# Optimization experiments

Measured on AMD Instinct MI355X. Metric: run time of the kernel, lower is better.

## Reference

```python
import jax, jax.numpy as jnp
import numpy as np

B, N, DIM = 4, 4096, 768
H = 12
DH = DIM // H          # 64
S = 16                 # num_segments
M = N // S             # 256 segment_len
SCALE = DH ** -0.5


def setup_inputs() -> dict:
    key = jax.random.key(0)
    ks = jax.random.split(key, 7)
    std = DIM ** -0.5
    return {
        "x": jax.random.normal(ks[0], (B, N, DIM), dtype=jnp.float32),
        "Wq": jax.random.normal(ks[1], (DIM, DIM), dtype=jnp.float32) * std,
        "Wkv": jax.random.normal(ks[2], (DIM, DIM), dtype=jnp.float32) * std,
        "Wo": jax.random.normal(ks[3], (DIM, DIM), dtype=jnp.float32) * std,
        "bo": jax.random.normal(ks[4], (DIM,), dtype=jnp.float32) * 0.02,
        "Wo0": jax.random.normal(ks[5], (DIM, DIM), dtype=jnp.float32) * std,
        "bo0": jax.random.normal(ks[6], (DIM,), dtype=jnp.float32) * 0.02,
    }


def _rotary_freqs(n, dh, dtype):
    # lucidrains RotaryEmbedding: inv_freq over even dims, emb = cat(freqs, freqs)
    inv_freq = 1.0 / (10000.0 ** (jnp.arange(0, dh, 2, dtype=jnp.float32) / dh))
    t = jnp.arange(n, dtype=jnp.float32)
    freqs = jnp.einsum("n,f->nf", t, inv_freq)           # (n, dh/2)
    return jnp.concatenate([freqs, freqs], axis=-1).astype(dtype)  # (n, dh)


def _rotate_half(t):
    # '... (j d) -> ... j d', j=2 ; (-x2, x1)
    x1, x2 = jnp.split(t, 2, axis=-1)
    return jnp.concatenate([-x2, x1], axis=-1)


def _apply_rotary(freqs, t):
    # freqs: (1, n, dh) broadcast over (bh, n, dh); rot_dim == dh here
    return t * jnp.cos(freqs) + _rotate_half(t) * jnp.sin(freqs)


def reference(x, Wq, Wkv, Wo, bo, Wo0, bo0):
    b, n, dim = x.shape
    q = x @ Wq            # (b, n, dim), bias-free
    kv = x @ Wkv          # shared K==V projection

    def to_heads(t):      # 'b n (h d) -> (b h) n d'
        return t.reshape(b, n, H, DH).transpose(0, 2, 1, 3).reshape(b * H, n, DH)

    q, kv = to_heads(q), to_heads(kv)

    freqs = _rotary_freqs(n, DH, x.dtype)[None, :, :]    # (1, n, dh)
    q = _apply_rotary(freqs, q)
    kv = _apply_rotary(freqs, kv)

    q = q * SCALE
    c = b * H
    qs = q.reshape(c, S, M, DH)
    kvs = kv.reshape(c, S, M, DH)

    # adjacent-segment KV windows: segment t attends to [t-1, t] for t>=1
    kvs_ccs = jnp.concatenate([kvs[:, :-1], kvs[:, 1:]], axis=2)  # (c, S-1, 2M, dh)
    qs_ccs = qs[:, 1:]                                            # (c, S-1, M, dh)

    lsim = jnp.einsum("csmd,csnd->csmn", qs_ccs, kvs_ccs)         # (c, S-1, M, 2M)
    attn1 = jax.nn.softmax(lsim, axis=-1)
    out1 = jnp.einsum("csmn,csnd->csmd", attn1, kvs_ccs)          # (c, S-1, M, dh)

    # global (self) attention within first segment
    q0, kv0 = qs[:, 0], kvs[:, 0]                                 # (c, M, dh)
    sim0 = jnp.einsum("cmd,cnd->cmn", q0, kv0)
    attn0 = jax.nn.softmax(sim0, axis=-1)
    out0 = jnp.einsum("cmn,cnd->cmd", attn0, kv0)                 # (c, M, dh)

    def merge_heads(t, nn):  # '(b h) nn d -> b nn (h d)'
        return t.reshape(b, H, nn, DH).transpose(0, 2, 1, 3).reshape(b, nn, H * DH)

    out_1 = merge_heads(out1.reshape(c, (S - 1) * M, DH), (S - 1) * M)
    out_0 = merge_heads(out0, M)

    out_1o = out_1 @ Wo + bo
    out_0o = out_0 @ Wo0 + bo0
    return jnp.concatenate([out_0o, out_1o], axis=1)              # (b, n, dim)
```

## Files before the change

### kernel.cpp

```cpp
#include <hip/hip_runtime.h>
#include <hip/hip_bf16.h>


typedef float f32x4 __attribute__((ext_vector_type(4)));
typedef short bf16x8 __attribute__((ext_vector_type(8)));

#define DEV static __device__ __forceinline__

DEV short f2bf(float f) {
  union { __hip_bfloat16 h; unsigned short u; } cv;
  cv.h = __float2bfloat16(f);
  return (short)cv.u;
}

DEV f32x4 fz4() { f32x4 z = {0.f, 0.f, 0.f, 0.f}; return z; }

DEV void gload16(const void* g, void* l) {
  __builtin_amdgcn_global_load_lds((const __attribute__((address_space(1))) void*)g,
                                   (__attribute__((address_space(3))) void*)l, 16, 0, 0);
}

__global__ void __launch_bounds__(256) k_rope(float* __restrict__ cosT,
                                              float* __restrict__ sinT) {
  int idx = blockIdx.x * 256 + threadIdx.x;
  int pos = idx >> 5, jm = idx & 31;
  float invf = exp2f(-(float)jm * (13.287712379549449f / 32.0f));
  float th = (float)pos * invf;
  cosT[idx] = cosf(th);
  sinT[idx] = sinf(th);
}

__global__ void __launch_bounds__(256) k_cvtx(const float* __restrict__ x,
                                              short* __restrict__ xb) {
  int i = (blockIdx.x * 256 + threadIdx.x) * 8;
  float4 a = *(const float4*)(x + i);
  float4 b = *(const float4*)(x + i + 4);
  bf16x8 v;
  v[0] = f2bf(a.x); v[1] = f2bf(a.y); v[2] = f2bf(a.z); v[3] = f2bf(a.w);
  v[4] = f2bf(b.x); v[5] = f2bf(b.y); v[6] = f2bf(b.z); v[7] = f2bf(b.w);
  *(bf16x8*)(xb + i) = v;
}

__global__ void __launch_bounds__(256) k_transw(const float* __restrict__ Wq,
                                                const float* __restrict__ Wkv,
                                                const float* __restrict__ Wo,
                                                const float* __restrict__ Wo0,
                                                short* __restrict__ WtQKV,
                                                short* __restrict__ WtO) {
  __shared__ float t[64][65];
  int z = blockIdx.z;
  const float* src = (z == 0) ? Wq : (z == 1) ? Wkv : (z == 2) ? Wo : Wo0;
  short* dst = (z < 2) ? (WtQKV + (size_t)z * (768 * 768))
                       : (WtO + (size_t)(z - 2) * (768 * 768));
  int k0 = blockIdx.x * 64, j0 = blockIdx.y * 64;
  int tc = threadIdx.x & 63, tr = threadIdx.x >> 6;
#pragma unroll
  for (int i = 0; i < 16; i++) {
    int r = i * 4 + tr;
    t[tc][r] = src[(size_t)(k0 + r) * 768 + j0 + tc];
  }
  __syncthreads();
#pragma unroll
  for (int i = 0; i < 16; i++) {
    int r = i * 4 + tr;
    dst[(size_t)(j0 + r) * 768 + k0 + tc] = f2bf(t[r][tc]);
  }
}

__global__ void __launch_bounds__(256, 2) k_gemm_qkv(
    const short* __restrict__ xb, const short* __restrict__ Wt,
    const float* __restrict__ cosT, const float* __restrict__ sinT,
    short* __restrict__ Qb, short* __restrict__ KVb) {
  __shared__ short Al[128 * 32];
  __shared__ short Bl[128 * 32];
  int r0 = blockIdx.x * 128;
  int cb = blockIdx.y;
  bool isQ = cb < 6;
  int cbl = isQ ? cb : cb - 6;
  const short* W = Wt + (isQ ? (size_t)0 : (size_t)(768 * 768));
  int j0 = cbl * 128;
  int tid = threadIdx.x, lane = tid & 63, wid = tid >> 6;
  int wr = wid >> 1, wc = wid & 1;
  int l15 = lane & 15, lg = lane >> 4;

  f32x4 acc[4][4];
#pragma unroll
  for (int i = 0; i < 4; i++)
#pragma unroll
    for (int j = 0; j < 4; j++) acc[i][j] = fz4();

  for (int kt = 0; kt < 24; kt++) {
    int k0 = kt * 32;
#pragma unroll
    for (int i = 0; i < 2; i++) {
      int g = i * 256 + tid;
      int row = g >> 2, oct = g & 3;
      gload16(xb + (size_t)(r0 + row) * 768 + k0 + oct * 8, &Al[(i * 256 + wid * 64) * 8]);
      gload16(W + (size_t)(j0 + row) * 768 + k0 + oct * 8, &Bl[(i * 256 + wid * 64) * 8]);
    }
    __syncthreads();
    bf16x8 af[4], bfr[4];
#pragma unroll
    for (int mr = 0; mr < 4; mr++)
      af[mr] = *(const bf16x8*)&Al[(wr * 64 + mr * 16 + l15) * 32 + lg * 8];
#pragma unroll
    for (int nc = 0; nc < 4; nc++)
      bfr[nc] = *(const bf16x8*)&Bl[(wc * 64 + nc * 16 + l15) * 32 + lg * 8];
#pragma unroll
    for (int mr = 0; mr < 4; mr++)
#pragma unroll
      for (int nc = 0; nc < 4; nc++)
        acc[mr][nc] = __builtin_amdgcn_mfma_f32_16x16x32_bf16(af[mr], bfr[nc], acc[mr][nc], 0, 0, 0);
    __syncthreads();
  }

  int h = 2 * cbl + wc;
  short* Ob = isQ ? Qb : KVb;
  float scl = isQ ? 0.18033688011112042f : 1.0f;
#pragma unroll
  for (int mr = 0; mr < 4; mr++) {
#pragma unroll
    for (int rg = 0; rg < 4; rg++) {
      int r = r0 + wr * 64 + mr * 16 + lg * 4 + rg;
      int b = r >> 12, pos = r & 4095;
      const float* cT = cosT + pos * 32;
      const float* sT = sinT + pos * 32;
      float c0 = cT[l15], s0 = sT[l15];
      float c1 = cT[16 + l15], s1 = sT[16 + l15];
      float v0 = acc[mr][0][rg], v1 = acc[mr][1][rg];
      float v2 = acc[mr][2][rg], v3 = acc[mr][3][rg];
      size_t base = ((size_t)((b * 12 + h) * 4096 + pos)) * 64 + l15;
      Ob[base]      = f2bf((v0 * c0 - v2 * s0) * scl);
      Ob[base + 16] = f2bf((v1 * c1 - v3 * s1) * scl);
      Ob[base + 32] = f2bf((v2 * c0 + v0 * s0) * scl);
      Ob[base + 48] = f2bf((v3 * c1 + v1 * s1) * scl);
    }
  }
}

__global__ void __launch_bounds__(256) k_transkv(const short* __restrict__ KVb,
                                                 short* __restrict__ KVt) {
  __shared__ short T[64][72];
  int c = blockIdx.x;
  int pt = blockIdx.y;
  int t = threadIdx.x;
  int ch = t & 7, rr = t >> 3;
#pragma unroll
  for (int i = 0; i < 2; i++) {
    int p = rr + i * 32;
    bf16x8 v = *(const bf16x8*)&KVb[((size_t)c * 4096 + pt * 64 + p) * 64 + ch * 8];
    *(bf16x8*)&T[p][ch * 8] = v;
  }
  __syncthreads();
#pragma unroll
  for (int i = 0; i < 2; i++) {
    int d = rr + i * 32;
    bf16x8 v;
#pragma unroll
    for (int j = 0; j < 8; j++) {
      int cc = ch * 8 + j;
      int g = cc >> 5, sig = cc & 31;
      int p = g * 32 + 4 * (sig >> 3) + (sig & 3) + 16 * ((sig >> 2) & 1);
      v[j] = T[p][d];
    }
    *(bf16x8*)&KVt[((size_t)c * 64 + d) * 4096 + pt * 64 + ch * 8] = v;
  }
}

#define STAGE(buf, kk0)                                                        \
  {                                                                            \
    _Pragma("unroll") for (int i = 0; i < 2; i++) {                            \
      gload16(KVc + (size_t)((kk0) + i * 32 + krow) * 128 + ksrccol,           \
              (char*)Kl[buf] + i * 4096 + wid * 1024);                         \
      gload16(KVtc + ((size_t)(i * 32 + krow) * 4096 + (kk0)) * 2 + ksrccol,   \
              (char*)Vl[buf] + i * 4096 + wid * 1024);                         \
    }                                                                          \
  }

__global__ void __launch_bounds__(256, 4) k_attn(const short* __restrict__ Qb,
                                                 const short* __restrict__ KVbp,
                                                 const short* __restrict__ KVtp,
                                                 short* __restrict__ AO) {
  __shared__ short Kl[2][4096];
  __shared__ short Vl[2][4096];
  int bid = blockIdx.x;
  int orig = (bid & 7) * 192 + (bid >> 3);
  int c = orig >> 5;
  int e = orig & 31;
  int s = (e < 2) ? 0 : ((e - 2) >> 1) + 1;
  int qh = (e < 2) ? e : (e - 2) & 1;
  int NC = (s == 0) ? 4 : 8;
  int Kbase = (s == 0) ? 0 : (s - 1) * 256;

  int tid = threadIdx.x, lane = tid & 63, wid = tid >> 6;
  int l15 = lane & 15, lg = lane >> 4;
  const char* KVc = (const char*)(KVbp + (size_t)c * 4096 * 64);
  const char* KVtc = (const char*)(KVtp + (size_t)c * 64 * 4096);

  int krow = tid >> 3;
  int ksrccol = ((tid & 7) * 16) ^ ((krow & 7) << 4);
  int swz = (l15 & 7) << 4;

  int q0 = s * 256 + qh * 128 + wid * 32;
  bf16x8 qf[2][2];
#pragma unroll
  for (int qt = 0; qt < 2; qt++) {
    const short* Qr = Qb + ((size_t)c * 4096 + q0 + qt * 16 + l15) * 64 + lg * 8;
    qf[qt][0] = *(const bf16x8*)Qr;
    qf[qt][1] = *(const bf16x8*)(Qr + 32);
  }

  const f32x4 mi = {-32.f, -32.f, -32.f, -32.f};
  bf16x8 ones;
#pragma unroll
  for (int j = 0; j < 8; j++) ones[j] = (short)0x3F80;

  f32x4 oacc[2][4];
  f32x4 lacc[2];
#pragma unroll
  for (int qt = 0; qt < 2; qt++) {
    lacc[qt] = fz4();
#pragma unroll
    for (int vt = 0; vt < 4; vt++) oacc[qt][vt] = fz4();
  }

  STAGE(0, Kbase)
  for (int ch = 0; ch < NC; ch++) {
    int cb = ch & 1;
    __syncthreads();
    if (ch + 1 < NC) STAGE(cb ^ 1, Kbase + (ch + 1) * 64)
    const char* Kb_ = (const char*)Kl[cb];
    const char* Vb_ = (const char*)Vl[cb];
#pragma unroll
    for (int u = 0; u < 2; u++) {
      f32x4 z[2][2];
#pragma unroll
      for (int t2 = 0; t2 < 2; t2++) {
        const char* Kp = Kb_ + ((2 * u + t2) * 16 + l15) * 128;
        bf16x8 kf0 = *(const bf16x8*)(Kp + ((lg * 16) ^ swz));
        bf16x8 kf1 = *(const bf16x8*)(Kp + ((64 + lg * 16) ^ swz));
        __builtin_amdgcn_s_setprio(1);
#pragma unroll
        for (int qt = 0; qt < 2; qt++) {
          f32x4 zz = __builtin_amdgcn_mfma_f32_16x16x32_bf16(kf0, qf[qt][0], mi, 0, 0, 0);
          zz = __builtin_amdgcn_mfma_f32_16x16x32_bf16(kf1, qf[qt][1], zz, 0, 0, 0);
          z[qt][t2] = zz;
        }
        __builtin_amdgcn_s_setprio(0);
      }
      bf16x8 pf[2];
#pragma unroll
      for (int qt = 0; qt < 2; qt++) {
#pragma unroll
        for (int t2 = 0; t2 < 2; t2++)
#pragma unroll
          for (int r = 0; r < 4; r++)
            pf[qt][t2 * 4 + r] = f2bf(exp2f(z[qt][t2][r]));
      }
      bf16x8 vf[4];
#pragma unroll
      for (int vt = 0; vt < 4; vt++)
        vf[vt] = *(const bf16x8*)(Vb_ + (vt * 16 + l15) * 128 +
                                  ((u * 64 + lg * 16) ^ swz));
      __builtin_amdgcn_s_setprio(1);
#pragma unroll
      for (int qt = 0; qt < 2; qt++) {
#pragma unroll
        for (int vt = 0; vt < 4; vt++)
          oacc[qt][vt] = __builtin_amdgcn_mfma_f32_16x16x32_bf16(pf[qt], vf[vt], oacc[qt][vt], 0, 0, 0);
        lacc[qt] = __builtin_amdgcn_mfma_f32_16x16x32_bf16(pf[qt], ones, lacc[qt], 0, 0, 0);
      }
      __builtin_amdgcn_s_setprio(0);
    }
  }

  int bq = c / 12, hh = c % 12;
#pragma unroll
  for (int qt = 0; qt < 2; qt++) {
    float rinv[4];
#pragma unroll
    for (int r = 0; r < 4; r++) rinv[r] = 1.0f / lacc[qt][r];
#pragma unroll
    for (int vt = 0; vt < 4; vt++)
#pragma unroll
      for (int r = 0; r < 4; r++) {
        size_t row = (size_t)bq * 4096 + q0 + qt * 16 + lg * 4 + r;
        AO[row * 768 + hh * 64 + vt * 16 + l15] = f2bf(oacc[qt][vt][r] * rinv[r]);
      }
  }
}

__global__ void __launch_bounds__(256, 2) k_gemm_out(
    const short* __restrict__ AO, const short* __restrict__ Wt,
    const float* __restrict__ bo, const float* __restrict__ bo0,
    float* __restrict__ out) {
  __shared__ short Al[128 * 32];
  __shared__ short Bl[128 * 32];
  int r0 = blockIdx.x * 128;
  int j0 = blockIdx.y * 128;
  bool o0sel = (r0 & 4095) < 256;
  const short* W = Wt + (o0sel ? (size_t)1 : (size_t)0) * (768 * 768);
  const float* bias = o0sel ? bo0 : bo;
  int tid = threadIdx.x, lane = tid & 63, wid = tid >> 6;
  int wr = wid >> 1, wc = wid & 1;
  int l15 = lane & 15, lg = lane >> 4;

  f32x4 acc[4][4];
#pragma unroll
  for (int i = 0; i < 4; i++)
#pragma unroll
    for (int j = 0; j < 4; j++) acc[i][j] = fz4();

  for (int kt = 0; kt < 24; kt++) {
    int k0 = kt * 32;
#pragma unroll
    for (int i = 0; i < 2; i++) {
      int g = i * 256 + tid;
      int row = g >> 2, oct = g & 3;
      gload16(AO + (size_t)(r0 + row) * 768 + k0 + oct * 8, &Al[(i * 256 + wid * 64) * 8]);
      gload16(W + (size_t)(j0 + row) * 768 + k0 + oct * 8, &Bl[(i * 256 + wid * 64) * 8]);
    }
    __syncthreads();
    bf16x8 af[4], bfr[4];
#pragma unroll
    for (int mr = 0; mr < 4; mr++)
      af[mr] = *(const bf16x8*)&Al[(wr * 64 + mr * 16 + l15) * 32 + lg * 8];
#pragma unroll
    for (int nc = 0; nc < 4; nc++)
      bfr[nc] = *(const bf16x8*)&Bl[(wc * 64 + nc * 16 + l15) * 32 + lg * 8];
#pragma unroll
    for (int mr = 0; mr < 4; mr++)
#pragma unroll
      for (int nc = 0; nc < 4; nc++)
        acc[mr][nc] = __builtin_amdgcn_mfma_f32_16x16x32_bf16(af[mr], bfr[nc], acc[mr][nc], 0, 0, 0);
    __syncthreads();
  }

  float bs[4];
#pragma unroll
  for (int nc = 0; nc < 4; nc++) bs[nc] = bias[j0 + wc * 64 + nc * 16 + l15];
#pragma unroll
  for (int mr = 0; mr < 4; mr++)
#pragma unroll
    for (int rg = 0; rg < 4; rg++) {
      size_t r = (size_t)r0 + wr * 64 + mr * 16 + lg * 4 + rg;
      float* op = out + r * 768 + j0 + wc * 64 + l15;
      op[0]  = acc[mr][0][rg] + bs[0];
      op[16] = acc[mr][1][rg] + bs[1];
      op[32] = acc[mr][2][rg] + bs[2];
      op[48] = acc[mr][3][rg] + bs[3];
    }
}

extern "C" void kernel_launch(void* const* d_in, const int* in_sizes, int n_in,
                              void* d_out, int out_size, void* d_ws, size_t ws_size,
                              hipStream_t stream) {
  (void)in_sizes; (void)n_in; (void)out_size; (void)ws_size;
  const float* x   = (const float*)d_in[0];
  const float* Wq  = (const float*)d_in[1];
  const float* Wkv = (const float*)d_in[2];
  const float* Wo  = (const float*)d_in[3];
  const float* bo  = (const float*)d_in[4];
  const float* Wo0 = (const float*)d_in[5];
  const float* bo0 = (const float*)d_in[6];
  float* out = (float*)d_out;

  char* ws = (char*)d_ws;
  short* xb    = (short*)(ws + 0);
  short* AO    = xb;
  short* Qb    = (short*)(ws + 25165824);
  short* KVb   = (short*)(ws + 50331648);
  short* KVt   = (short*)(ws + 75497472);
  short* WtQKV = (short*)(ws + 75497472);
  float* cosT  = (float*)(ws + 77856768);
  float* sinT  = (float*)(ws + 78381056);
  short* WtO   = (short*)(ws + 100663296);

  k_rope<<<512, 256, 0, stream>>>(cosT, sinT);
  k_cvtx<<<6144, 256, 0, stream>>>(x, xb);
  k_transw<<<dim3(12, 12, 4), 256, 0, stream>>>(Wq, Wkv, Wo, Wo0, WtQKV, WtO);
  k_gemm_qkv<<<dim3(128, 12), 256, 0, stream>>>(xb, WtQKV, cosT, sinT, Qb, KVb);
  k_transkv<<<dim3(48, 64), 256, 0, stream>>>(KVb, KVt);
  k_attn<<<1536, 256, 0, stream>>>(Qb, KVb, KVt, AO);
  k_gemm_out<<<dim3(128, 6), 256, 0, stream>>>(AO, WtO, bo, bo0, out);
}
```

Measured before the change: 154.5 us.

## Double-buffer and swizzle LDS tiles in QKV and output projection GEMMs

Both projection GEMMs now use two LDS buffers per operand. The next K-tile is loaded asynchronously while MFMAs run on the current one, which removes one barrier per iteration. Columns in LDS are XOR-swizzled by row to reduce bank conflicts on the fragment reads, and launch bounds ask for 4 blocks per CU to raise occupancy. The cost is doubled LDS per block and possible register pressure from the higher occupancy target.

```diff
diff --git a/kernel.cpp b/kernel.cpp
--- a/kernel.cpp
+++ b/kernel.cpp
@@ -67,21 +67,35 @@
   }
 }
 
-__global__ void __launch_bounds__(256, 2) k_gemm_qkv(
+#define QSTAGE(Abuf, Bbuf, Abase, Bbase, kt)                                   \
+  {                                                                            \
+    _Pragma("unroll") for (int i = 0; i < 2; i++) {                            \
+      int rowi = i * 64 + wid * 16 + (lane >> 2);                              \
+      int cci = (kt) * 64 + ((((lane & 3) ^ (rowi & 3)) << 4));                \
+      gload16((Abase) + (size_t)(r0 + rowi) * 1536 + cci,                      \
+              (char*)(Abuf) + i * 4096 + wid * 1024);                          \
+      gload16((Bbase) + (size_t)(j0 + rowi) * 1536 + cci,                      \
+              (char*)(Bbuf) + i * 4096 + wid * 1024);                          \
+    }                                                                          \
+  }
+
+__global__ void __launch_bounds__(256, 4) k_gemm_qkv(
     const short* __restrict__ xb, const short* __restrict__ Wt,
     const float* __restrict__ cosT, const float* __restrict__ sinT,
     short* __restrict__ Qb, short* __restrict__ KVb) {
-  __shared__ short Al[128 * 32];
-  __shared__ short Bl[128 * 32];
+  __shared__ short Al[2][4096];
+  __shared__ short Bl[2][4096];
   int r0 = blockIdx.x * 128;
-  int cb = blockIdx.y;
-  bool isQ = cb < 6;
-  int cbl = isQ ? cb : cb - 6;
-  const short* W = Wt + (isQ ? (size_t)0 : (size_t)(768 * 768));
+  int cbk = blockIdx.y;
+  bool isQ = cbk < 6;
+  int cbl = isQ ? cbk : cbk - 6;
+  const char* Ab = (const char*)xb;
+  const char* Bb = (const char*)(Wt + (isQ ? (size_t)0 : (size_t)(768 * 768)));
   int j0 = cbl * 128;
   int tid = threadIdx.x, lane = tid & 63, wid = tid >> 6;
   int wr = wid >> 1, wc = wid & 1;
   int l15 = lane & 15, lg = lane >> 4;
+  int rsw = (l15 & 3) << 4;
 
   f32x4 acc[4][4];
 #pragma unroll
@@ -89,29 +103,25 @@
 #pragma unroll
     for (int j = 0; j < 4; j++) acc[i][j] = fz4();
 
+  QSTAGE(Al[0], Bl[0], Ab, Bb, 0)
   for (int kt = 0; kt < 24; kt++) {
-    int k0 = kt * 32;
-#pragma unroll
-    for (int i = 0; i < 2; i++) {
-      int g = i * 256 + tid;
-      int row = g >> 2, oct = g & 3;
-      gload16(xb + (size_t)(r0 + row) * 768 + k0 + oct * 8, &Al[(i * 256 + wid * 64) * 8]);
-      gload16(W + (size_t)(j0 + row) * 768 + k0 + oct * 8, &Bl[(i * 256 + wid * 64) * 8]);
-    }
+    int cb = kt & 1;
     __syncthreads();
+    if (kt + 1 < 24) QSTAGE(Al[cb ^ 1], Bl[cb ^ 1], Ab, Bb, kt + 1)
+    const char* Ac = (const char*)Al[cb];
+    const char* Bc = (const char*)Bl[cb];
     bf16x8 af[4], bfr[4];
 #pragma unroll
     for (int mr = 0; mr < 4; mr++)
-      af[mr] = *(const bf16x8*)&Al[(wr * 64 + mr * 16 + l15) * 32 + lg * 8];
+      af[mr] = *(const bf16x8*)(Ac + (wr * 64 + mr * 16 + l15) * 64 + ((lg * 16) ^ rsw));
 #pragma unroll
     for (int nc = 0; nc < 4; nc++)
-      bfr[nc] = *(const bf16x8*)&Bl[(wc * 64 + nc * 16 + l15) * 32 + lg * 8];
+      bfr[nc] = *(const bf16x8*)(Bc + (wc * 64 + nc * 16 + l15) * 64 + ((lg * 16) ^ rsw));
 #pragma unroll
     for (int mr = 0; mr < 4; mr++)
 #pragma unroll
       for (int nc = 0; nc < 4; nc++)
         acc[mr][nc] = __builtin_amdgcn_mfma_f32_16x16x32_bf16(af[mr], bfr[nc], acc[mr][nc], 0, 0, 0);
-    __syncthreads();
   }
 
   int h = 2 * cbl + wc;
@@ -290,20 +300,22 @@
   }
 }
 
-__global__ void __launch_bounds__(256, 2) k_gemm_out(
+__global__ void __launch_bounds__(256, 4) k_gemm_out(
     const short* __restrict__ AO, const short* __restrict__ Wt,
     const float* __restrict__ bo, const float* __restrict__ bo0,
     float* __restrict__ out) {
-  __shared__ short Al[128 * 32];
-  __shared__ short Bl[128 * 32];
+  __shared__ short Al[2][4096];
+  __shared__ short Bl[2][4096];
   int r0 = blockIdx.x * 128;
   int j0 = blockIdx.y * 128;
   bool o0sel = (r0 & 4095) < 256;
-  const short* W = Wt + (o0sel ? (size_t)1 : (size_t)0) * (768 * 768);
+  const char* Ab = (const char*)AO;
+  const char* Bb = (const char*)(Wt + (o0sel ? (size_t)1 : (size_t)0) * (768 * 768));
   const float* bias = o0sel ? bo0 : bo;
   int tid = threadIdx.x, lane = tid & 63, wid = tid >> 6;
   int wr = wid >> 1, wc = wid & 1;
   int l15 = lane & 15, lg = lane >> 4;
+  int rsw = (l15 & 3) << 4;
 
   f32x4 acc[4][4];
 #pragma unroll
@@ -311,29 +323,25 @@
 #pragma unroll
     for (int j = 0; j < 4; j++) acc[i][j] = fz4();
 
+  QSTAGE(Al[0], Bl[0], Ab, Bb, 0)
   for (int kt = 0; kt < 24; kt++) {
-    int k0 = kt * 32;
-#pragma unroll
-    for (int i = 0; i < 2; i++) {
-      int g = i * 256 + tid;
-      int row = g >> 2, oct = g & 3;
-      gload16(AO + (size_t)(r0 + row) * 768 + k0 + oct * 8, &Al[(i * 256 + wid * 64) * 8]);
-      gload16(W + (size_t)(j0 + row) * 768 + k0 + oct * 8, &Bl[(i * 256 + wid * 64) * 8]);
-    }
+    int cb = kt & 1;
     __syncthreads();
+    if (kt + 1 < 24) QSTAGE(Al[cb ^ 1], Bl[cb ^ 1], Ab, Bb, kt + 1)
+    const char* Ac = (const char*)Al[cb];
+    const char* Bc = (const char*)Bl[cb];
     bf16x8 af[4], bfr[4];
 #pragma unroll
     for (int mr = 0; mr < 4; mr++)
-      af[mr] = *(const bf16x8*)&Al[(wr * 64 + mr * 16 + l15) * 32 + lg * 8];
+      af[mr] = *(const bf16x8*)(Ac + (wr * 64 + mr * 16 + l15) * 64 + ((lg * 16) ^ rsw));
 #pragma unroll
     for (int nc = 0; nc < 4; nc++)
-      bfr[nc] = *(const bf16x8*)&Bl[(wc * 64 + nc * 16 + l15) * 32 + lg * 8];
+      bfr[nc] = *(const bf16x8*)(Bc + (wc * 64 + nc * 16 + l15) * 64 + ((lg * 16) ^ rsw));
 #pragma unroll
     for (int mr = 0; mr < 4; mr++)
 #pragma unroll
       for (int nc = 0; nc < 4; nc++)
         acc[mr][nc] = __builtin_amdgcn_mfma_f32_16x16x32_bf16(af[mr], bfr[nc], acc[mr][nc], 0, 0, 0);
-    __syncthreads();
   }
 
   float bs[4];
```

Result: no change. 155.2 us (+0.5%).
